# Optimization experiments

Measured on AMD Instinct MI355X. Metric: run time of the kernel, lower is better.

Reference implementation:

```python
import jax, jax.numpy as jnp
import numpy as np
import math

LN_EPS = 1e-5

def setup_inputs() -> dict:
    key = jax.random.key(0)
    ks = jax.random.split(key, 8)
    B, S, D = 2, 2048, 2048
    sc = 1.0 / math.sqrt(D)
    return {
        "x": jax.random.normal(ks[0], (B, S, D), dtype=jnp.float32),
        "Wq": jax.random.normal(ks[1], (D, D), dtype=jnp.float32) * sc,
        "bq": jnp.zeros((D,), jnp.float32),
        "Wk": jax.random.normal(ks[2], (D, D), dtype=jnp.float32) * sc,
        "bk": jnp.zeros((D,), jnp.float32),
        "Wv": jax.random.normal(ks[3], (D, D), dtype=jnp.float32) * sc,
        "bv": jnp.zeros((D,), jnp.float32),
        "Wo": jax.random.normal(ks[4], (D, D), dtype=jnp.float32) * sc,
        "bo": jnp.zeros((D,), jnp.float32),
        "gamma": jnp.ones((D,), jnp.float32),
        "beta": jnp.zeros((D,), jnp.float32),
        "num_heads": 16,
    }

def reference(x, Wq, bq, Wk, bk, Wv, bv, Wo, bo, gamma, beta, num_heads):
    B, S, D = x.shape
    H = num_heads
    Dh = D // H
    # projections (torch Linear: y = x W^T + b; here W stored as [in,out])
    q = (x @ Wq + bq).reshape(B, S, H, Dh).transpose(0, 2, 1, 3)  # [B,H,S,Dh]
    k = (x @ Wk + bk).reshape(B, S, H, Dh).transpose(0, 2, 1, 3)
    v = (x @ Wv + bv).reshape(B, S, H, Dh).transpose(0, 2, 1, 3)
    scores = jnp.einsum("bhqd,bhkd->bhqk", q, k) / jnp.sqrt(jnp.asarray(Dh, x.dtype))
    causal = jnp.tril(jnp.ones((S, S), bool))  # [S,S]
    scores = jnp.where(causal[None, None], scores, -jnp.inf)
    # original subtracts row-max then softmax == stable softmax
    attn = jax.nn.softmax(scores, axis=-1)
    ctx = jnp.einsum("bhqk,bhkd->bhqd", attn, v)
    ctx = ctx.transpose(0, 2, 1, 3).reshape(B, S, D)
    attn_out = ctx @ Wo + bo
    y = attn_out + x
    mu = jnp.mean(y, axis=-1, keepdims=True)
    var = jnp.mean((y - mu) ** 2, axis=-1, keepdims=True)
    ln = gamma * (y - mu) * jax.lax.rsqrt(var + LN_EPS) + beta
    return (ln, attn_out, k, v)
```

## Files before the change

### kernel.cpp

```cpp
#include <hip/hip_runtime.h>
#include <hip/hip_bf16.h>
#include <math.h>
#include <stdint.h>

typedef __bf16 bf16;
typedef __bf16 bf16x4 __attribute__((ext_vector_type(4)));
typedef __bf16 bf16x8 __attribute__((ext_vector_type(8)));
typedef float f32x4 __attribute__((ext_vector_type(4)));

#define D_MODEL 2048
#define SEQ     2048
#define NHEADS  16
#define DH      128

__device__ __forceinline__ void async_copy16(const bf16* g, bf16* l) {
    typedef const unsigned int __attribute__((address_space(1))) gu32;
    typedef unsigned int __attribute__((address_space(3))) lu32;
    __builtin_amdgcn_global_load_lds((gu32*)g, (lu32*)(unsigned int)(unsigned long long)(l),
                                     16, 0, 0);
}

__global__ __launch_bounds__(256)
void convert_x_kernel(const float* __restrict__ x, bf16* __restrict__ xb)
{
    int i = blockIdx.x * 256 + threadIdx.x;
    float4 v = ((const float4*)x)[i];
    bf16x4 o;
    o[0] = (bf16)v.x; o[1] = (bf16)v.y; o[2] = (bf16)v.z; o[3] = (bf16)v.w;
    ((bf16x4*)xb)[i] = o;
}

__global__ __launch_bounds__(256)
void transpose_w_kernel(const float* __restrict__ Wq, const float* __restrict__ Wk,
                        const float* __restrict__ Wv, const float* __restrict__ Wo,
                        bf16* __restrict__ WTbase)
{
    const int z = blockIdx.z;
    const float* __restrict__ W = (z == 0) ? Wq : (z == 1) ? Wk : (z == 2) ? Wv : Wo;
    bf16* __restrict__ Wt = WTbase + (size_t)z * (D_MODEL * D_MODEL);
    const int n0 = blockIdx.x * 64, k0 = blockIdx.y * 64;
    const int tid = threadIdx.x;
    __shared__ bf16 Tl[64][68];

#pragma unroll
    for (int i = 0; i < 4; ++i) {
        int idx = tid + i * 256;
        int kr = idx >> 4, nc = (idx & 15) * 4;
        float4 w = *(const float4*)&W[(size_t)(k0 + kr) * D_MODEL + n0 + nc];
        Tl[nc + 0][kr] = (bf16)w.x;
        Tl[nc + 1][kr] = (bf16)w.y;
        Tl[nc + 2][kr] = (bf16)w.z;
        Tl[nc + 3][kr] = (bf16)w.w;
    }
    __syncthreads();
#pragma unroll
    for (int i = 0; i < 4; ++i) {
        int idx = tid + i * 256;
        int nr = idx >> 4, kc = (idx & 15) * 4;
        *(bf16x4*)&Wt[(size_t)(n0 + nr) * D_MODEL + k0 + kc] = *(const bf16x4*)&Tl[nr][kc];
    }
}

__global__ __launch_bounds__(256)
void transpose_v_kernel(const float* __restrict__ V, bf16* __restrict__ Vt)
{
    const int s0 = blockIdx.x * 64, d0 = blockIdx.y * 64, bh = blockIdx.z;
    const float* __restrict__ Vb = V + (size_t)bh * SEQ * DH;
    bf16* __restrict__ Vtb = Vt + (size_t)bh * DH * SEQ;
    const int tid = threadIdx.x;
    __shared__ bf16 Tl[64][68];

#pragma unroll
    for (int i = 0; i < 4; ++i) {
        int idx = tid + i * 256;
        int sr = idx >> 4, dc = (idx & 15) * 4;
        float4 v = *(const float4*)&Vb[(size_t)(s0 + sr) * DH + d0 + dc];
        Tl[dc + 0][sr] = (bf16)v.x;
        Tl[dc + 1][sr] = (bf16)v.y;
        Tl[dc + 2][sr] = (bf16)v.z;
        Tl[dc + 3][sr] = (bf16)v.w;
    }
    __syncthreads();
#pragma unroll
    for (int i = 0; i < 4; ++i) {
        int idx = tid + i * 256;
        int dr = idx >> 4, sc = (idx & 15) * 4;
        *(bf16x4*)&Vtb[(size_t)(d0 + dr) * SEQ + s0 + sc] = *(const bf16x4*)&Tl[dr][sc];
    }
}

__device__ __forceinline__ void gemm128x256_core(const bf16* __restrict__ A,
                                                 const bf16* __restrict__ Bt,
                                                 int bm, int bn,
                                                 bf16* lds,
                                                 f32x4 acc[4][4])
{
    const int tid = threadIdx.x;
    const int wave = tid >> 6, lane = tid & 63, quad = lane >> 4, l16 = lane & 15;
    const int wr = wave >> 2, wc = wave & 3;

    const bf16* pA[2]; int dA[2];
#pragma unroll
    for (int j = 0; j < 2; ++j) {
        const int f = j * 8 + wave;
        pA[j] = A + (size_t)(bm * 128 + (f >> 1) * 16 + l16) * D_MODEL + (f & 1) * 32 + quad * 8;
        dA[j] = f * 512 + lane * 8;
    }
    const bf16* pB[4]; int dB[4];
#pragma unroll
    for (int i = 0; i < 4; ++i) {
        const int f = (i >> 1) * 16 + (i & 1) * 8 + wave;
        pB[i] = Bt + (size_t)(bn * 256 + (f >> 1) * 16 + l16) * D_MODEL + (f & 1) * 32 + quad * 8;
        dB[i] = f * 512 + lane * 8;
    }

    auto stA = [&](int p, int kt) {
#pragma unroll
        for (int j = 0; j < 2; ++j)
            async_copy16(pA[j] + kt * 64, lds + p * 24576 + dA[j]);
    };
    auto stB = [&](int p, int kt, int h) {
#pragma unroll
        for (int j = 0; j < 2; ++j)
            async_copy16(pB[h * 2 + j] + kt * 64, lds + p * 24576 + 8192 + dB[h * 2 + j]);
    };

    stA(0, 0); stB(0, 0, 0); stB(0, 0, 1); stB(1, 1, 0); stB(1, 1, 1);
    asm volatile("s_waitcnt vmcnt(4)" ::: "memory");
    __builtin_amdgcn_s_barrier();

    for (int t = 0; t < 32; ++t) {
        const int p = t & 1;
        const bf16* Ab = lds + p * 24576;
        const bf16* Bb = Ab + 8192;
        const int tn1 = (t + 1 < 31) ? t + 1 : 31;
        const int tn2 = (t + 2 < 31) ? t + 2 : 31;

        bf16x8 bfr[4][2], af[2][2];

#pragma unroll
        for (int mi = 0; mi < 2; ++mi)
#pragma unroll
            for (int kk = 0; kk < 2; ++kk)
                af[mi][kk] = *(const bf16x8*)(Ab + ((wr * 4 + mi) * 2 + kk) * 512 + lane * 8);
#pragma unroll
        for (int n = 0; n < 4; ++n)
#pragma unroll
            for (int kk = 0; kk < 2; ++kk)
                bfr[n][kk] = *(const bf16x8*)(Bb + ((wc * 4 + n) * 2 + kk) * 512 + lane * 8);
        stA(p ^ 1, tn1);
        __builtin_amdgcn_s_barrier();
        asm volatile("s_waitcnt lgkmcnt(0)" ::: "memory");
        __builtin_amdgcn_sched_barrier(0);
        __builtin_amdgcn_s_setprio(1);
#pragma unroll
        for (int mi = 0; mi < 2; ++mi)
#pragma unroll
            for (int n = 0; n < 4; ++n)
#pragma unroll
                for (int kk = 0; kk < 2; ++kk)
                    acc[mi][n] = __builtin_amdgcn_mfma_f32_16x16x32_bf16(
                        af[mi][kk], bfr[n][kk], acc[mi][n], 0, 0, 0);
        __builtin_amdgcn_s_setprio(0);
        __builtin_amdgcn_s_barrier();

#pragma unroll
        for (int mi = 0; mi < 2; ++mi)
#pragma unroll
            for (int kk = 0; kk < 2; ++kk)
                af[mi][kk] = *(const bf16x8*)(Ab + ((wr * 4 + 2 + mi) * 2 + kk) * 512 + lane * 8);
        stB(p, tn2, 0); stB(p, tn2, 1);
        __builtin_amdgcn_s_barrier();
        asm volatile("s_waitcnt lgkmcnt(0)" ::: "memory");
        __builtin_amdgcn_sched_barrier(0);
        __builtin_amdgcn_s_setprio(1);
#pragma unroll
        for (int mi = 0; mi < 2; ++mi)
#pragma unroll
            for (int n = 0; n < 4; ++n)
#pragma unroll
                for (int kk = 0; kk < 2; ++kk)
                    acc[2 + mi][n] = __builtin_amdgcn_mfma_f32_16x16x32_bf16(
                        af[mi][kk], bfr[n][kk], acc[2 + mi][n], 0, 0, 0);
        __builtin_amdgcn_s_setprio(0);
        asm volatile("s_waitcnt vmcnt(4)" ::: "memory");
        __builtin_amdgcn_s_barrier();
    }
    asm volatile("s_waitcnt vmcnt(0)" ::: "memory");
}

__global__ __launch_bounds__(512, 2)
void gemm_qkv_kernel(const bf16* __restrict__ A, const bf16* __restrict__ WT,
                     const float* __restrict__ bq, const float* __restrict__ bk,
                     const float* __restrict__ bv,
                     bf16* __restrict__ qout, float* __restrict__ kout,
                     bf16* __restrict__ kb16, float* __restrict__ vout)
{
    __shared__ bf16 lds[49152];
    const int id = blockIdx.x;
    const int swz = (id & 7) * 96 + (id >> 3);
    const int bm = swz & 31, bn = swz >> 5;

    f32x4 acc[4][4] = {};
    gemm128x256_core(A, WT, bm, bn, lds, acc);

    const int tid = threadIdx.x;
    const int wave = tid >> 6, lane = tid & 63, quad = lane >> 4, l16 = lane & 15;
    const int wr = wave >> 2, wc = wave & 3;
    const int z = bn >> 3;
    const float* __restrict__ bias = (z == 0) ? bq : (z == 1) ? bk : bv;

#pragma unroll
    for (int a = 0; a < 4; ++a) {
#pragma unroll
        for (int n = 0; n < 4; ++n) {
#pragma unroll
            for (int r = 0; r < 4; ++r) {
                int m  = bm * 128 + wr * 64 + a * 16 + quad * 4 + r;
                int nl = (bn & 7) * 256 + wc * 64 + n * 16 + l16;
                float val = acc[a][n][r] + bias[nl];
                int b = m >> 11, s = m & (SEQ - 1);
                int h = nl >> 7, dh = nl & (DH - 1);
                size_t off = ((size_t)(b * NHEADS + h) * SEQ + s) * DH + dh;
                if (z == 0) {
                    qout[off] = (bf16)val;
                } else if (z == 1) {
                    kout[off] = val;
                    kb16[off] = (bf16)val;
                } else {
                    vout[off] = val;
                }
            }
        }
    }
}

__global__ __launch_bounds__(512, 2)
void gemm_out_kernel(const bf16* __restrict__ A, const bf16* __restrict__ Bt,
                     const float* __restrict__ bias, float* __restrict__ out)
{
    __shared__ bf16 lds[49152];
    const int id = blockIdx.x;
    const int swz = (id & 7) * 32 + (id >> 3);
    const int bm = swz & 31, bn = swz >> 5;

    f32x4 acc[4][4] = {};
    gemm128x256_core(A, Bt, bm, bn, lds, acc);

    const int tid = threadIdx.x;
    const int wave = tid >> 6, lane = tid & 63, quad = lane >> 4, l16 = lane & 15;
    const int wr = wave >> 2, wc = wave & 3;

#pragma unroll
    for (int a = 0; a < 4; ++a) {
#pragma unroll
        for (int n = 0; n < 4; ++n) {
#pragma unroll
            for (int r = 0; r < 4; ++r) {
                int m  = bm * 128 + wr * 64 + a * 16 + quad * 4 + r;
                int nn = bn * 256 + wc * 64 + n * 16 + l16;
                out[(size_t)m * D_MODEL + nn] = acc[a][n][r] + bias[nn];
            }
        }
    }
}

__global__ __launch_bounds__(256, 4)
void attn_kernel(const bf16* __restrict__ Q, const bf16* __restrict__ K,
                 const bf16* __restrict__ Vt, bf16* __restrict__ ctx)
{
    const int id = blockIdx.x;
    const int p  = id & 511;
    const int bh = p >> 4;
    const int j  = p & 15;
    const int qb = (id >> 9) ? j : (31 - j);

    const int tid = threadIdx.x;
    const int wave = tid >> 6, lane = tid & 63, quad = lane >> 4, l16 = lane & 15;

    __shared__ bf16 Ks[64 * 128];
    __shared__ bf16 VsT[128 * 64];
    __shared__ bf16 Ps[4 * 16 * 64];
    char* const ksb = (char*)Ks;
    char* const vsb = (char*)VsT;
    char* const psb = (char*)Ps + wave * 2048;

    const bf16* qsrc = Q + ((size_t)bh * SEQ + (size_t)qb * 64 + wave * 16 + l16) * DH;
    bf16x8 qf[4];
#pragma unroll
    for (int dd = 0; dd < 4; ++dd)
        qf[dd] = *(const bf16x8*)&qsrc[dd * 32 + quad * 8];

    f32x4 o[8] = {};
    float m_i[4], l_i[4];
#pragma unroll
    for (int r = 0; r < 4; ++r) { m_i[r] = -INFINITY; l_i[r] = 0.f; }

    const float scale = 0.08838834764831845f;
    const bf16* ksrc0 = K + (size_t)bh * SEQ * DH;
    const bf16* vsrc0 = Vt + (size_t)bh * DH * SEQ;

    for (int kb = 0; kb <= qb; ++kb) {
        __syncthreads();

        {
            const char* kg = (const char*)(ksrc0 + (size_t)(kb * 64) * DH);
#pragma unroll
            for (int i = 0; i < 4; ++i) {
                int seg = i * 4 + wave;
                int row = seg * 4 + (lane >> 4);
                int colb = (lane & 15) * 16;
                const char* src = kg + row * 256 + (colb ^ ((row & 7) << 4));
                async_copy16((const bf16*)src, (bf16*)(ksb + seg * 1024));
            }
            const char* vg = (const char*)(vsrc0 + kb * 64);
#pragma unroll
            for (int i = 0; i < 4; ++i) {
                int seg = i * 4 + wave;
                int d = seg * 8 + (lane >> 3);
                int colb = (lane & 7) * 16;
                const char* src = vg + (size_t)d * (SEQ * 2) + (colb ^ ((d & 7) << 4));
                async_copy16((const bf16*)src, (bf16*)(vsb + seg * 1024));
            }
        }
        __syncthreads();

        float pvals[4][4];
#pragma unroll
        for (int t = 0; t < 4; ++t) {
            f32x4 s = {};
            const int row = t * 16 + l16;
            const int swz = (row & 7) << 4;
#pragma unroll
            for (int dd = 0; dd < 4; ++dd) {
                bf16x8 b = *(const bf16x8*)(ksb + row * 256 + ((dd * 64 + quad * 16) ^ swz));
                s = __builtin_amdgcn_mfma_f32_16x16x32_bf16(qf[dd], b, s, 0, 0, 0);
            }
#pragma unroll
            for (int r = 0; r < 4; ++r) pvals[t][r] = s[r];
        }

        const bool diag = (kb == qb);
#pragma unroll
        for (int r = 0; r < 4; ++r) {
            int qrow = qb * 64 + wave * 16 + quad * 4 + r;
            float mx = -INFINITY;
#pragma unroll
            for (int t = 0; t < 4; ++t) {
                float s = pvals[t][r] * scale;
                int kcol = kb * 64 + t * 16 + l16;
                if (diag && kcol > qrow) s = -INFINITY;
                pvals[t][r] = s;
                mx = fmaxf(mx, s);
            }
#pragma unroll
            for (int off = 1; off < 16; off <<= 1)
                mx = fmaxf(mx, __shfl_xor(mx, off, 64));
            float mnew = fmaxf(m_i[r], mx);
            float alpha = __expf(m_i[r] - mnew);
            m_i[r] = mnew;
            float rs = 0.f;
#pragma unroll
            for (int t = 0; t < 4; ++t) {
                float pexp = __expf(pvals[t][r] - mnew);
                pvals[t][r] = pexp;
                rs += pexp;
            }
#pragma unroll
            for (int off = 1; off < 16; off <<= 1)
                rs += __shfl_xor(rs, off, 64);
            l_i[r] = l_i[r] * alpha + rs;
#pragma unroll
            for (int dt = 0; dt < 8; ++dt) o[dt][r] *= alpha;
        }

#pragma unroll
        for (int t = 0; t < 4; ++t)
#pragma unroll
            for (int r = 0; r < 4; ++r) {
                int row = quad * 4 + r;
                *(bf16*)(psb + row * 128 + (((t * 16 + l16) * 2) ^ ((row & 7) << 4))) =
                    (bf16)pvals[t][r];
            }

        bf16x8 pa[2];
#pragma unroll
        for (int kk2 = 0; kk2 < 2; ++kk2)
            pa[kk2] = *(const bf16x8*)(psb + l16 * 128 +
                                       ((kk2 * 64 + quad * 16) ^ ((l16 & 7) << 4)));
#pragma unroll
        for (int dt = 0; dt < 8; ++dt) {
            const int row = dt * 16 + l16;
            const int swz = (row & 7) << 4;
#pragma unroll
            for (int kk2 = 0; kk2 < 2; ++kk2) {
                bf16x8 b = *(const bf16x8*)(vsb + row * 128 + ((kk2 * 64 + quad * 16) ^ swz));
                o[dt] = __builtin_amdgcn_mfma_f32_16x16x32_bf16(pa[kk2], b, o[dt], 0, 0, 0);
            }
        }
    }

    const int b = bh >> 4, h = bh & (NHEADS - 1);
    float inv_l[4];
#pragma unroll
    for (int r = 0; r < 4; ++r) inv_l[r] = 1.0f / l_i[r];
#pragma unroll
    for (int dt = 0; dt < 8; ++dt) {
#pragma unroll
        for (int r = 0; r < 4; ++r) {
            int s = qb * 64 + wave * 16 + quad * 4 + r;
            int d = dt * 16 + l16;
            ctx[((size_t)(b * SEQ + s)) * D_MODEL + h * DH + d] = (bf16)(o[dt][r] * inv_l[r]);
        }
    }
}

__global__ __launch_bounds__(256)
void ln_kernel(const float* __restrict__ attn, const float* __restrict__ x,
               const float* __restrict__ gamma, const float* __restrict__ beta,
               float* __restrict__ ln)
{
    const int row = blockIdx.x;
    const int tid = threadIdx.x;
    const int wave = tid >> 6, lane = tid & 63;
    const float* a  = attn + (size_t)row * D_MODEL;
    const float* xr = x    + (size_t)row * D_MODEL;

    float4 y4[2];
    float sum = 0.f, sumsq = 0.f;
#pragma unroll
    for (int i = 0; i < 2; ++i) {
        int c = (tid + i * 256) * 4;
        float4 av = *(const float4*)&a[c];
        float4 xv = *(const float4*)&xr[c];
        float4 y;
        y.x = av.x + xv.x; y.y = av.y + xv.y; y.z = av.z + xv.z; y.w = av.w + xv.w;
        y4[i] = y;
        sum   += y.x + y.y + y.z + y.w;
        sumsq += y.x * y.x + y.y * y.y + y.z * y.z + y.w * y.w;
    }
#pragma unroll
    for (int off = 1; off < 64; off <<= 1) {
        sum   += __shfl_xor(sum, off, 64);
        sumsq += __shfl_xor(sumsq, off, 64);
    }
    __shared__ float rsum[4], rsumsq[4];
    if (lane == 0) { rsum[wave] = sum; rsumsq[wave] = sumsq; }
    __syncthreads();
    float tot = 0.f, tot2 = 0.f;
#pragma unroll
    for (int i = 0; i < 4; ++i) { tot += rsum[i]; tot2 += rsumsq[i]; }
    const float mu  = tot * (1.0f / D_MODEL);
    const float var = tot2 * (1.0f / D_MODEL) - mu * mu;
    const float rstd = rsqrtf(var + 1e-5f);

#pragma unroll
    for (int i = 0; i < 2; ++i) {
        int c = (tid + i * 256) * 4;
        float4 gv = *(const float4*)&gamma[c];
        float4 bv = *(const float4*)&beta[c];
        float4 y = y4[i];
        float4 r;
        r.x = gv.x * (y.x - mu) * rstd + bv.x;
        r.y = gv.y * (y.y - mu) * rstd + bv.y;
        r.z = gv.z * (y.z - mu) * rstd + bv.z;
        r.w = gv.w * (y.w - mu) * rstd + bv.w;
        *(float4*)&ln[(size_t)row * D_MODEL + c] = r;
    }
}

extern "C" void kernel_launch(void* const* d_in, const int* in_sizes, int n_in,
                              void* d_out, int out_size, void* d_ws, size_t ws_size,
                              hipStream_t stream)
{
    const float* x     = (const float*)d_in[0];
    const float* Wq    = (const float*)d_in[1];
    const float* bq    = (const float*)d_in[2];
    const float* Wk    = (const float*)d_in[3];
    const float* bk    = (const float*)d_in[4];
    const float* Wv    = (const float*)d_in[5];
    const float* bv    = (const float*)d_in[6];
    const float* Wo    = (const float*)d_in[7];
    const float* bo    = (const float*)d_in[8];
    const float* gamma = (const float*)d_in[9];
    const float* beta  = (const float*)d_in[10];

    float* out      = (float*)d_out;
    float* ln       = out;
    float* attn_out = out + 8388608;
    float* kout     = out + 16777216;
    float* vout     = out + 25165824;

    bf16* wsb  = (bf16*)d_ws;
    bf16* xb   = wsb;
    bf16* WT   = wsb + 8388608;
    bf16* qws  = wsb + 25165824;
    bf16* kb16 = wsb + 33554432;
    bf16* vT   = wsb + 41943040;
    bf16* ctx  = wsb + 50331648;

    convert_x_kernel<<<8192, 256, 0, stream>>>(x, xb);
    transpose_w_kernel<<<dim3(32, 32, 4), 256, 0, stream>>>(Wq, Wk, Wv, Wo, WT);
    gemm_qkv_kernel<<<dim3(768), 512, 0, stream>>>(xb, WT, bq, bk, bv,
                                                    qws, kout, kb16, vout);
    transpose_v_kernel<<<dim3(32, 2, 32), 256, 0, stream>>>(vout, vT);
    attn_kernel<<<dim3(1024), 256, 0, stream>>>(qws, kb16, vT, ctx);
    gemm_out_kernel<<<dim3(256), 512, 0, stream>>>(ctx, WT + 3 * (size_t)(D_MODEL * D_MODEL),
                                                    bo, attn_out);
    ln_kernel<<<4096, 256, 0, stream>>>(attn_out, x, gamma, beta, ln);
}
```

Before: 595.9 us.

## Use 256x192 QKV GEMM tiles and fuse V transpose into epilogue

Replaces the 128x256 tile core for the QKV projection with a new 256x192 tile core. It uses a different double-buffer and prefetch schedule and launches 512 blocks instead of 768, so each block does more work and A/B reuse per tile rises. The epilogue now writes the bf16 transposed V directly, which removes the separate transpose_v kernel launch and its re-read of the fp32 V output. The trade-offs are more LDS per block and more accumulator registers, which may cut occupancy. The fused transposed-V stores are 8-byte strided writes.

Measured after the change: 557.6 us. -6.4%, faster.

```diff
diff --git a/kernel.cpp b/kernel.cpp
--- a/kernel.cpp
+++ b/kernel.cpp
@@ -61,32 +61,103 @@
     }
 }
 
-__global__ __launch_bounds__(256)
-void transpose_v_kernel(const float* __restrict__ V, bf16* __restrict__ Vt)
-{
-    const int s0 = blockIdx.x * 64, d0 = blockIdx.y * 64, bh = blockIdx.z;
-    const float* __restrict__ Vb = V + (size_t)bh * SEQ * DH;
-    bf16* __restrict__ Vtb = Vt + (size_t)bh * DH * SEQ;
-    const int tid = threadIdx.x;
-    __shared__ bf16 Tl[64][68];
-
-#pragma unroll
-    for (int i = 0; i < 4; ++i) {
-        int idx = tid + i * 256;
-        int sr = idx >> 4, dc = (idx & 15) * 4;
-        float4 v = *(const float4*)&Vb[(size_t)(s0 + sr) * DH + d0 + dc];
-        Tl[dc + 0][sr] = (bf16)v.x;
-        Tl[dc + 1][sr] = (bf16)v.y;
-        Tl[dc + 2][sr] = (bf16)v.z;
-        Tl[dc + 3][sr] = (bf16)v.w;
-    }
-    __syncthreads();
-#pragma unroll
-    for (int i = 0; i < 4; ++i) {
-        int idx = tid + i * 256;
-        int dr = idx >> 4, sc = (idx & 15) * 4;
-        *(bf16x4*)&Vtb[(size_t)(d0 + dr) * SEQ + s0 + sc] = *(const bf16x4*)&Tl[dr][sc];
-    }
+__device__ __forceinline__ void gemm256x192_core(const bf16* __restrict__ A,
+                                                 const bf16* __restrict__ Bt,
+                                                 int bm, int bn,
+                                                 bf16* lds,
+                                                 f32x4 acc[8][3])
+{
+    const int tid = threadIdx.x;
+    const int wave = tid >> 6, lane = tid & 63, quad = lane >> 4, l16 = lane & 15;
+    const int wr = wave >> 2, wc = wave & 3;
+
+    const bf16* pA[4]; int dA[4];
+#pragma unroll
+    for (int h = 0; h < 2; ++h)
+#pragma unroll
+        for (int j = 0; j < 2; ++j) {
+            const int f = h * 16 + j * 8 + wave;
+            pA[h * 2 + j] = A + (size_t)(bm * 256 + (f >> 1) * 16 + l16) * D_MODEL
+                              + (f & 1) * 32 + quad * 8;
+            dA[h * 2 + j] = f * 512 + lane * 8;
+        }
+    const bf16* pB[3]; int dB[3];
+#pragma unroll
+    for (int part = 0; part < 3; ++part) {
+        const int f = part * 8 + wave;
+        pB[part] = Bt + (size_t)(bn * 192 + (f >> 1) * 16 + l16) * D_MODEL
+                      + (f & 1) * 32 + quad * 8;
+        dB[part] = 16384 + f * 512 + lane * 8;
+    }
+
+    auto stA = [&](int p, int kt, int h) {
+#pragma unroll
+        for (int j = 0; j < 2; ++j)
+            async_copy16(pA[h * 2 + j] + kt * 64, lds + p * 28672 + dA[h * 2 + j]);
+    };
+    auto stB = [&](int p, int kt, int part) {
+        async_copy16(pB[part] + kt * 64, lds + p * 28672 + dB[part]);
+    };
+
+    stA(0, 0, 0); stA(0, 0, 1);
+    stB(0, 0, 0); stB(0, 0, 1); stB(0, 0, 2);
+    stB(1, 1, 0); stB(1, 1, 1); stB(1, 1, 2);
+    asm volatile("s_waitcnt vmcnt(3)" ::: "memory");
+    __builtin_amdgcn_s_barrier();
+
+    for (int t = 0; t < 32; ++t) {
+        const int p = t & 1;
+        const bf16* Ab = lds + p * 28672;
+        const bf16* Bb = Ab + 16384;
+        const int tn1 = (t + 1 < 31) ? t + 1 : 31;
+        const int tn2 = (t + 2 < 31) ? t + 2 : 31;
+        bf16x8 bfr[3][2];
+#pragma unroll
+        for (int q = 0; q < 4; ++q) {
+            bf16x8 af[2][2];
+#pragma unroll
+            for (int mi = 0; mi < 2; ++mi)
+#pragma unroll
+                for (int kk = 0; kk < 2; ++kk) {
+                    const int mt = wr * 8 + 2 * q + mi;
+                    af[mi][kk] = *(const bf16x8*)(Ab + (mt * 2 + kk) * 512 + lane * 8);
+                }
+            if (q == 0) {
+#pragma unroll
+                for (int n = 0; n < 3; ++n)
+#pragma unroll
+                    for (int kk = 0; kk < 2; ++kk) {
+                        const int nt = wc * 3 + n;
+                        bfr[n][kk] = *(const bf16x8*)(Bb + (nt * 2 + kk) * 512 + lane * 8);
+                    }
+                stA(p ^ 1, tn1, 0);
+            } else if (q == 1) {
+                stA(p ^ 1, tn1, 1);
+                stB(p, tn2, 0);
+            } else if (q == 2) {
+                stB(p, tn2, 1);
+            } else {
+                stB(p, tn2, 2);
+            }
+
+            __builtin_amdgcn_s_barrier();
+            asm volatile("s_waitcnt lgkmcnt(0)" ::: "memory");
+            __builtin_amdgcn_sched_barrier(0);
+            __builtin_amdgcn_s_setprio(1);
+#pragma unroll
+            for (int mi = 0; mi < 2; ++mi)
+#pragma unroll
+                for (int n = 0; n < 3; ++n)
+#pragma unroll
+                    for (int kk = 0; kk < 2; ++kk)
+                        acc[2 * q + mi][n] = __builtin_amdgcn_mfma_f32_16x16x32_bf16(
+                            af[mi][kk], bfr[n][kk], acc[2 * q + mi][n], 0, 0, 0);
+            __builtin_amdgcn_s_setprio(0);
+            if (q == 3) asm volatile("s_waitcnt vmcnt(3)" ::: "memory");
+            __builtin_amdgcn_s_barrier();
+        }
+    }
+    asm volatile("s_waitcnt vmcnt(0)" ::: "memory");
 }
 
 __device__ __forceinline__ void gemm128x256_core(const bf16* __restrict__ A,
@@ -194,33 +265,38 @@
                      const float* __restrict__ bq, const float* __restrict__ bk,
                      const float* __restrict__ bv,
                      bf16* __restrict__ qout, float* __restrict__ kout,
-                     bf16* __restrict__ kb16, float* __restrict__ vout)
-{
-    __shared__ bf16 lds[49152];
+                     bf16* __restrict__ kb16, float* __restrict__ vout,
+                     bf16* __restrict__ vtout)
+{
+    __shared__ bf16 lds[57344];
     const int id = blockIdx.x;
-    const int swz = (id & 7) * 96 + (id >> 3);
-    const int bm = swz & 31, bn = swz >> 5;
-
-    f32x4 acc[4][4] = {};
-    gemm128x256_core(A, WT, bm, bn, lds, acc);
+    const int swz = (id & 7) * 64 + (id >> 3);
+    const int bm = swz >> 5, bn = swz & 31;
+
+    f32x4 acc[8][3] = {};
+    gemm256x192_core(A, WT, bm, bn, lds, acc);
 
     const int tid = threadIdx.x;
     const int wave = tid >> 6, lane = tid & 63, quad = lane >> 4, l16 = lane & 15;
     const int wr = wave >> 2, wc = wave & 3;
-    const int z = bn >> 3;
-    const float* __restrict__ bias = (z == 0) ? bq : (z == 1) ? bk : bv;
-
-#pragma unroll
-    for (int a = 0; a < 4; ++a) {
-#pragma unroll
-        for (int n = 0; n < 4; ++n) {
+
+#pragma unroll
+    for (int a = 0; a < 8; ++a) {
+#pragma unroll
+        for (int n = 0; n < 3; ++n) {
+            const int col0 = bn * 192 + wc * 48 + n * 16;
+            const int z = col0 >> 11;
+            const float* __restrict__ bias = (z == 0) ? bq : (z == 1) ? bk : bv;
+            const int nl = (col0 & 2047) + l16;
+            const int h = nl >> 7, dh = nl & (DH - 1);
+            const int m0 = bm * 256 + wr * 128 + a * 16 + quad * 4;
+            const int b0 = m0 >> 11, s0 = m0 & (SEQ - 1);
+            bf16x4 vt4;
 #pragma unroll
             for (int r = 0; r < 4; ++r) {
-                int m  = bm * 128 + wr * 64 + a * 16 + quad * 4 + r;
-                int nl = (bn & 7) * 256 + wc * 64 + n * 16 + l16;
+                int m = m0 + r;
                 float val = acc[a][n][r] + bias[nl];
                 int b = m >> 11, s = m & (SEQ - 1);
-                int h = nl >> 7, dh = nl & (DH - 1);
                 size_t off = ((size_t)(b * NHEADS + h) * SEQ + s) * DH + dh;
                 if (z == 0) {
                     qout[off] = (bf16)val;
@@ -229,7 +305,12 @@
                     kb16[off] = (bf16)val;
                 } else {
                     vout[off] = val;
+                    vt4[r] = (bf16)val;
                 }
+            }
+            if (z == 2) {
+                size_t voff = ((size_t)(b0 * NHEADS + h) * DH + dh) * SEQ + s0;
+                *(bf16x4*)&vtout[voff] = vt4;
             }
         }
     }
@@ -501,9 +582,8 @@
 
     convert_x_kernel<<<8192, 256, 0, stream>>>(x, xb);
     transpose_w_kernel<<<dim3(32, 32, 4), 256, 0, stream>>>(Wq, Wk, Wv, Wo, WT);
-    gemm_qkv_kernel<<<dim3(768), 512, 0, stream>>>(xb, WT, bq, bk, bv,
-                                                    qws, kout, kb16, vout);
-    transpose_v_kernel<<<dim3(32, 2, 32), 256, 0, stream>>>(vout, vT);
+    gemm_qkv_kernel<<<dim3(512), 512, 0, stream>>>(xb, WT, bq, bk, bv,
+                                                    qws, kout, kb16, vout, vT);
     attn_kernel<<<dim3(1024), 256, 0, stream>>>(qws, kb16, vT, ctx);
     gemm_out_kernel<<<dim3(256), 512, 0, stream>>>(ctx, WT + 3 * (size_t)(D_MODEL * D_MODEL),
                                                     bo, attn_out);
```
